# Optimization experiments

Measured on AMD Instinct MI355X. Metric: run time of the kernel, lower is better.

## Reference

```python
import jax, jax.numpy as jnp
import numpy as np

N_NODES = 100000
N_EDGES = 1600000
IN_C = 64
OUT_C = 64
BN_EPS = 1e-5


def setup_inputs() -> dict:
    key = jax.random.key(0)
    k1, k2, k3, k4 = jax.random.split(key, 4)
    x = jax.random.normal(k1, (N_NODES, IN_C), dtype=jnp.float32)
    edge_index = jax.random.randint(k2, (2, N_EDGES), 0, N_NODES, dtype=jnp.int64)
    # GCNConv linear: weight [out, in], bias [out] (PyG default has bias=True)
    W = jax.random.normal(k3, (OUT_C, IN_C), dtype=jnp.float32) / np.sqrt(IN_C)
    b = jax.random.normal(k4, (OUT_C,), dtype=jnp.float32) * 0.01
    # BatchNorm1d affine params
    gamma = jnp.ones((OUT_C,), dtype=jnp.float32)
    beta = jnp.zeros((OUT_C,), dtype=jnp.float32)
    return {"x": x, "edge_index": edge_index, "W": W, "b": b, "gamma": gamma, "beta": beta}


def reference(x, edge_index, W, b, gamma, beta):
    N = x.shape[0]
    # GCNConv: linear transform (no bias yet)
    h = x @ W.T  # [N, out]
    # add self-loops
    loop = jnp.arange(N, dtype=edge_index.dtype)
    src = jnp.concatenate([edge_index[0], loop])  # [E+N]
    dst = jnp.concatenate([edge_index[1], loop])
    # symmetric normalization: deg computed on destination (col)
    ones = jnp.ones(src.shape[0], dtype=h.dtype)
    deg = jax.ops.segment_sum(ones, dst, num_segments=N)  # [N]
    deg_inv_sqrt = jnp.where(deg > 0, jax.lax.rsqrt(deg), 0.0)
    norm = deg_inv_sqrt[src] * deg_inv_sqrt[dst]  # [E+N]
    # gather -> scale -> scatter-add aggregation
    msgs = h[src] * norm[:, None]  # [E+N, out] (dominant memory traffic)
    out = jax.ops.segment_sum(msgs, dst, num_segments=N) + b  # [N, out]
    # BatchNorm1d (training mode: biased batch statistics over nodes)
    mean = out.mean(axis=0)
    var = out.var(axis=0)  # biased, matching torch BN normalization
    y = (out - mean) * jax.lax.rsqrt(var + BN_EPS) * gamma + beta
    return jax.nn.relu(y)
```

## Files before the change

### kernel.cpp

```cpp
#include <hip/hip_runtime.h>
#include <math.h>

#define N_NODES 100000
#define N_EDGES 1600000
#define C 64
#define BN_EPS 1e-5f
#define SLOTS 48

#define WS_HP    0
#define WS_CNT   3200000
#define WS_STAT  3300000
#define WS_SLOT  3300128

#define NPART 8
#define PART_NODES (N_NODES / NPART)
#define NCHUNK 128
#define CHUNK_I4 (N_EDGES / 4 / NCHUNK)

static __device__ __forceinline__ unsigned short f2bf(float f) {
    unsigned u = __float_as_uint(f);
    unsigned r = 0x7FFFu + ((u >> 16) & 1u);
    return (unsigned short)((u + r) >> 16);
}
static __device__ __forceinline__ float bf2f(unsigned short h) {
    return __uint_as_float(((unsigned)h) << 16);
}

__global__ void r10_init(unsigned* __restrict__ cnt, float* __restrict__ stats) {
    int i = blockIdx.x * blockDim.x + threadIdx.x;
    if (i < N_NODES) cnt[i] = 0u;
    if (i < 128) stats[i] = 0.0f;
}

__global__ void r10_scatter(const int* __restrict__ ei, unsigned* __restrict__ cnt,
                            unsigned* __restrict__ slot) {
    const int p  = blockIdx.x & (NPART - 1);
    const int ch = blockIdx.x >> 3;
    const unsigned lo = (unsigned)(p * PART_NODES);
    const unsigned hi = lo + PART_NODES;
    const int4* d4 = reinterpret_cast<const int4*>(ei + N_EDGES);
    const int beg = ch * CHUNK_I4;
    const int end = beg + CHUNK_I4;
    for (int e = beg + threadIdx.x; e < end; e += 256) {
        int4 d = d4[e];
        unsigned dx = (unsigned)d.x, dy = (unsigned)d.y;
        unsigned dz = (unsigned)d.z, dw = (unsigned)d.w;
        if (dx >= lo && dx < hi) {
            unsigned s = (unsigned)ei[4 * e + 0];
            unsigned pos = atomicAdd(&cnt[dx], 1u);
            if (pos < SLOTS) slot[dx * SLOTS + pos] = s;
        }
        if (dy >= lo && dy < hi) {
            unsigned s = (unsigned)ei[4 * e + 1];
            unsigned pos = atomicAdd(&cnt[dy], 1u);
            if (pos < SLOTS) slot[dy * SLOTS + pos] = s;
        }
        if (dz >= lo && dz < hi) {
            unsigned s = (unsigned)ei[4 * e + 2];
            unsigned pos = atomicAdd(&cnt[dz], 1u);
            if (pos < SLOTS) slot[dz * SLOTS + pos] = s;
        }
        if (dw >= lo && dw < hi) {
            unsigned s = (unsigned)ei[4 * e + 3];
            unsigned pos = atomicAdd(&cnt[dw], 1u);
            if (pos < SLOTS) slot[dw * SLOTS + pos] = s;
        }
    }
}

__global__ void r10_mm(const float* __restrict__ x, const float* __restrict__ W,
                       const unsigned* __restrict__ cnt, unsigned short* __restrict__ hp) {
    __shared__ float Wt[64 * 64];
    __shared__ float X[16 * 64];
    const int tid = threadIdx.x;
    for (int i = tid; i < 64 * 64; i += 256)
        Wt[i] = W[((i & 63) << 6) + (i >> 6)];

    const int c = tid & 63;
    const int w = tid >> 6;
    const int nrow = tid >> 4;
    const int k4 = (tid & 15) << 2;
    const int ngroups = N_NODES / 16;

    for (int g = blockIdx.x; g < ngroups; g += gridDim.x) {
        const int base = g * 16;
        __syncthreads();
        *reinterpret_cast<float4*>(X + nrow * 64 + k4) =
            *reinterpret_cast<const float4*>(x + (base + nrow) * 64 + k4);
        __syncthreads();

        float acc0 = 0.f, acc1 = 0.f, acc2 = 0.f, acc3 = 0.f;
        #pragma unroll
        for (int k = 0; k < 64; k += 4) {
            float w0 = Wt[(k + 0) * 64 + c];
            float w1 = Wt[(k + 1) * 64 + c];
            float w2 = Wt[(k + 2) * 64 + c];
            float w3 = Wt[(k + 3) * 64 + c];
            float4 x0 = *reinterpret_cast<const float4*>(X + (w * 4 + 0) * 64 + k);
            float4 x1 = *reinterpret_cast<const float4*>(X + (w * 4 + 1) * 64 + k);
            float4 x2 = *reinterpret_cast<const float4*>(X + (w * 4 + 2) * 64 + k);
            float4 x3 = *reinterpret_cast<const float4*>(X + (w * 4 + 3) * 64 + k);
            acc0 += x0.x * w0 + x0.y * w1 + x0.z * w2 + x0.w * w3;
            acc1 += x1.x * w0 + x1.y * w1 + x1.z * w2 + x1.w * w3;
            acc2 += x2.x * w0 + x2.y * w1 + x2.z * w2 + x2.w * w3;
            acc3 += x3.x * w0 + x3.y * w1 + x3.z * w2 + x3.w * w3;
        }
        const int n0 = base + w * 4;
        hp[(n0 + 0) * 64 + c] = f2bf(acc0 * rsqrtf((float)(cnt[n0 + 0] + 1u)));
        hp[(n0 + 1) * 64 + c] = f2bf(acc1 * rsqrtf((float)(cnt[n0 + 1] + 1u)));
        hp[(n0 + 2) * 64 + c] = f2bf(acc2 * rsqrtf((float)(cnt[n0 + 2] + 1u)));
        hp[(n0 + 3) * 64 + c] = f2bf(acc3 * rsqrtf((float)(cnt[n0 + 3] + 1u)));
    }
}

__global__ void r10_agg(const unsigned* __restrict__ slot, const unsigned* __restrict__ cnt,
                        const unsigned short* __restrict__ hp, float* __restrict__ out,
                        float* __restrict__ stats) {
    __shared__ float ls[256], lq[256];
    const int tid = threadIdx.x;
    const int c = tid & 63;
    int wid = blockIdx.x * (blockDim.x >> 6) + (tid >> 6);
    const int nw = gridDim.x * (blockDim.x >> 6);
    float s = 0.0f, q = 0.0f;
    for (int n = wid; n < N_NODES; n += nw) {
        unsigned deg = cnt[n];
        int num = (deg > SLOTS) ? SLOTS : (int)deg;
        float dn = rsqrtf((float)(deg + 1u));
        float acc = bf2f(hp[n * 64 + c]);
        unsigned p = (c < num) ? slot[n * SLOTS + c] : 0u;
        int j = 0;
        for (; j + 8 <= num; j += 8) {
            unsigned s0 = __shfl(p, j + 0), s1 = __shfl(p, j + 1);
            unsigned s2 = __shfl(p, j + 2), s3 = __shfl(p, j + 3);
            unsigned s4 = __shfl(p, j + 4), s5 = __shfl(p, j + 5);
            unsigned s6 = __shfl(p, j + 6), s7 = __shfl(p, j + 7);
            float a0 = bf2f(hp[s0 * 64 + c]);
            float a1 = bf2f(hp[s1 * 64 + c]);
            float a2 = bf2f(hp[s2 * 64 + c]);
            float a3 = bf2f(hp[s3 * 64 + c]);
            float a4 = bf2f(hp[s4 * 64 + c]);
            float a5 = bf2f(hp[s5 * 64 + c]);
            float a6 = bf2f(hp[s6 * 64 + c]);
            float a7 = bf2f(hp[s7 * 64 + c]);
            acc += ((a0 + a1) + (a2 + a3)) + ((a4 + a5) + (a6 + a7));
        }
        for (; j + 4 <= num; j += 4) {
            unsigned s0 = __shfl(p, j + 0), s1 = __shfl(p, j + 1);
            unsigned s2 = __shfl(p, j + 2), s3 = __shfl(p, j + 3);
            float a0 = bf2f(hp[s0 * 64 + c]);
            float a1 = bf2f(hp[s1 * 64 + c]);
            float a2 = bf2f(hp[s2 * 64 + c]);
            float a3 = bf2f(hp[s3 * 64 + c]);
            acc += (a0 + a1) + (a2 + a3);
        }
        for (; j < num; ++j)
            acc += bf2f(hp[__shfl(p, j) * 64 + c]);
        float o = acc * dn;
        out[n * 64 + c] = o;
        s += o; q += o * o;
    }
    ls[tid] = s; lq[tid] = q;
    __syncthreads();
    if (tid < 64) {
        s = ls[tid] + ls[tid + 64] + ls[tid + 128] + ls[tid + 192];
        q = lq[tid] + lq[tid + 64] + lq[tid + 128] + lq[tid + 192];
        atomicAdd(&stats[tid], s);
        atomicAdd(&stats[64 + tid], q);
    }
}

__global__ void r10_bnrelu(float* __restrict__ out, const float* __restrict__ sum,
                           const float* __restrict__ sq, const float* __restrict__ gamma,
                           const float* __restrict__ beta) {
    int i = blockIdx.x * blockDim.x + threadIdx.x;
    const int st = gridDim.x * blockDim.x;
    const int c0 = (i & 15) << 2;
    float scl[4], sft[4];
    #pragma unroll
    for (int k = 0; k < 4; ++k) {
        float mean = sum[c0 + k] * (1.0f / N_NODES);
        float var  = sq[c0 + k] * (1.0f / N_NODES) - mean * mean;
        float inv  = rsqrtf(var + BN_EPS);
        scl[k] = gamma[c0 + k] * inv;
        sft[k] = beta[c0 + k] - mean * scl[k];
    }
    const int total4 = N_NODES * C / 4;
    for (; i < total4; i += st) {
        float4 v = reinterpret_cast<float4*>(out)[i];
        v.x = fmaxf(v.x * scl[0] + sft[0], 0.0f);
        v.y = fmaxf(v.y * scl[1] + sft[1], 0.0f);
        v.z = fmaxf(v.z * scl[2] + sft[2], 0.0f);
        v.w = fmaxf(v.w * scl[3] + sft[3], 0.0f);
        reinterpret_cast<float4*>(out)[i] = v;
    }
}

extern "C" void kernel_launch(void* const* d_in, const int* in_sizes, int n_in,
                              void* d_out, int out_size, void* d_ws, size_t ws_size,
                              hipStream_t stream) {
    const float* x     = (const float*)d_in[0];
    const int*   ei    = (const int*)d_in[1];
    const float* W     = (const float*)d_in[2];
    const float* gamma = (const float*)d_in[4];
    const float* beta  = (const float*)d_in[5];
    float* out = (float*)d_out;
    float*    wsf = (float*)d_ws;
    unsigned* wsu = (unsigned*)d_ws;

    unsigned short* hp = (unsigned short*)(wsf + WS_HP);
    unsigned* cnt   = wsu + WS_CNT;
    float*    stats = wsf + WS_STAT;
    unsigned* slot  = wsu + WS_SLOT;

    r10_init   <<<(N_NODES + 255) / 256, 256, 0, stream>>>(cnt, stats);
    r10_scatter<<<NPART * NCHUNK, 256, 0, stream>>>(ei, cnt, slot);
    r10_mm     <<<2048, 256, 0, stream>>>(x, W, cnt, hp);
    r10_agg    <<<4096, 256, 0, stream>>>(slot, cnt, hp, out, stats);
    r10_bnrelu <<<1024, 256, 0, stream>>>(out, stats, stats + 64, gamma, beta);
}
```

Before: 241.1 us.

## Gather two bf16 channels per lane across half-wave edge split in aggregation

The aggregation kernel now has each half of a wavefront process alternate neighbor edges, with each lane loading a 4-byte pair of bf16 channels instead of one 2-byte value. The two halves are then combined through shuffles. This halves the number of gather load instructions per edge and widens each access. Separately, the weight transpose in the matmul kernel gets a padded LDS layout with coalesced global reads, the output stores and loads in the final passes use nontemporal hints, and the bnrelu grid is doubled. The cost is extra shuffles and select operations per node, and a different floating-point summation order.

Measured after the change: 240.1 us. About the same (-0.4%).

```diff
diff --git a/kernel.cpp b/kernel.cpp
--- a/kernel.cpp
+++ b/kernel.cpp
@@ -17,6 +17,8 @@
 #define NCHUNK 128
 #define CHUNK_I4 (N_EDGES / 4 / NCHUNK)
 
+typedef float f4 __attribute__((ext_vector_type(4)));
+
 static __device__ __forceinline__ unsigned short f2bf(float f) {
     unsigned u = __float_as_uint(f);
     unsigned r = 0x7FFFu + ((u >> 16) & 1u);
@@ -26,13 +28,13 @@
     return __uint_as_float(((unsigned)h) << 16);
 }
 
-__global__ void r10_init(unsigned* __restrict__ cnt, float* __restrict__ stats) {
+__global__ void r20_init(unsigned* __restrict__ cnt, float* __restrict__ stats) {
     int i = blockIdx.x * blockDim.x + threadIdx.x;
     if (i < N_NODES) cnt[i] = 0u;
     if (i < 128) stats[i] = 0.0f;
 }
 
-__global__ void r10_scatter(const int* __restrict__ ei, unsigned* __restrict__ cnt,
+__global__ void r20_scatter(const int* __restrict__ ei, unsigned* __restrict__ cnt,
                             unsigned* __restrict__ slot) {
     const int p  = blockIdx.x & (NPART - 1);
     const int ch = blockIdx.x >> 3;
@@ -68,13 +70,15 @@
     }
 }
 
-__global__ void r10_mm(const float* __restrict__ x, const float* __restrict__ W,
+__global__ void r20_mm(const float* __restrict__ x, const float* __restrict__ W,
                        const unsigned* __restrict__ cnt, unsigned short* __restrict__ hp) {
-    __shared__ float Wt[64 * 64];
+    __shared__ float Wt[64 * 65];
     __shared__ float X[16 * 64];
     const int tid = threadIdx.x;
-    for (int i = tid; i < 64 * 64; i += 256)
-        Wt[i] = W[((i & 63) << 6) + (i >> 6)];
+    for (int i = tid; i < 64 * 64; i += 256) {
+        float v = W[i];
+        Wt[(i & 63) * 65 + (i >> 6)] = v;
+    }
 
     const int c = tid & 63;
     const int w = tid >> 6;
@@ -92,10 +96,10 @@
         float acc0 = 0.f, acc1 = 0.f, acc2 = 0.f, acc3 = 0.f;
         #pragma unroll
         for (int k = 0; k < 64; k += 4) {
-            float w0 = Wt[(k + 0) * 64 + c];
-            float w1 = Wt[(k + 1) * 64 + c];
-            float w2 = Wt[(k + 2) * 64 + c];
-            float w3 = Wt[(k + 3) * 64 + c];
+            float w0 = Wt[(k + 0) * 65 + c];
+            float w1 = Wt[(k + 1) * 65 + c];
+            float w2 = Wt[(k + 2) * 65 + c];
+            float w3 = Wt[(k + 3) * 65 + c];
             float4 x0 = *reinterpret_cast<const float4*>(X + (w * 4 + 0) * 64 + k);
             float4 x1 = *reinterpret_cast<const float4*>(X + (w * 4 + 1) * 64 + k);
             float4 x2 = *reinterpret_cast<const float4*>(X + (w * 4 + 2) * 64 + k);
@@ -113,50 +117,58 @@
     }
 }
 
-__global__ void r10_agg(const unsigned* __restrict__ slot, const unsigned* __restrict__ cnt,
+__global__ void r20_agg(const unsigned* __restrict__ slot, const unsigned* __restrict__ cnt,
                         const unsigned short* __restrict__ hp, float* __restrict__ out,
                         float* __restrict__ stats) {
     __shared__ float ls[256], lq[256];
     const int tid = threadIdx.x;
     const int c = tid & 63;
-    int wid = blockIdx.x * (blockDim.x >> 6) + (tid >> 6);
-    const int nw = gridDim.x * (blockDim.x >> 6);
+    const int half = c >> 5;
+    const int l2 = (c & 31) * 2;
+    int wid = blockIdx.x * 4 + (tid >> 6);
+    const int nw = gridDim.x * 4;
     float s = 0.0f, q = 0.0f;
     for (int n = wid; n < N_NODES; n += nw) {
         unsigned deg = cnt[n];
         int num = (deg > SLOTS) ? SLOTS : (int)deg;
         float dn = rsqrtf((float)(deg + 1u));
-        float acc = bf2f(hp[n * 64 + c]);
         unsigned p = (c < num) ? slot[n * SLOTS + c] : 0u;
+        float alo = 0.f, ahi = 0.f;
         int j = 0;
         for (; j + 8 <= num; j += 8) {
-            unsigned s0 = __shfl(p, j + 0), s1 = __shfl(p, j + 1);
-            unsigned s2 = __shfl(p, j + 2), s3 = __shfl(p, j + 3);
-            unsigned s4 = __shfl(p, j + 4), s5 = __shfl(p, j + 5);
-            unsigned s6 = __shfl(p, j + 6), s7 = __shfl(p, j + 7);
-            float a0 = bf2f(hp[s0 * 64 + c]);
-            float a1 = bf2f(hp[s1 * 64 + c]);
-            float a2 = bf2f(hp[s2 * 64 + c]);
-            float a3 = bf2f(hp[s3 * 64 + c]);
-            float a4 = bf2f(hp[s4 * 64 + c]);
-            float a5 = bf2f(hp[s5 * 64 + c]);
-            float a6 = bf2f(hp[s6 * 64 + c]);
-            float a7 = bf2f(hp[s7 * 64 + c]);
-            acc += ((a0 + a1) + (a2 + a3)) + ((a4 + a5) + (a6 + a7));
-        }
-        for (; j + 4 <= num; j += 4) {
-            unsigned s0 = __shfl(p, j + 0), s1 = __shfl(p, j + 1);
-            unsigned s2 = __shfl(p, j + 2), s3 = __shfl(p, j + 3);
-            float a0 = bf2f(hp[s0 * 64 + c]);
-            float a1 = bf2f(hp[s1 * 64 + c]);
-            float a2 = bf2f(hp[s2 * 64 + c]);
-            float a3 = bf2f(hp[s3 * 64 + c]);
-            acc += (a0 + a1) + (a2 + a3);
-        }
-        for (; j < num; ++j)
-            acc += bf2f(hp[__shfl(p, j) * 64 + c]);
-        float o = acc * dn;
-        out[n * 64 + c] = o;
+            unsigned r0e = __shfl(p, j + 0), r0o = __shfl(p, j + 1);
+            unsigned r1e = __shfl(p, j + 2), r1o = __shfl(p, j + 3);
+            unsigned r2e = __shfl(p, j + 4), r2o = __shfl(p, j + 5);
+            unsigned r3e = __shfl(p, j + 6), r3o = __shfl(p, j + 7);
+            unsigned r0 = half ? r0o : r0e;
+            unsigned r1 = half ? r1o : r1e;
+            unsigned r2 = half ? r2o : r2e;
+            unsigned r3 = half ? r3o : r3e;
+            ushort2 v0 = *reinterpret_cast<const ushort2*>(hp + r0 * 64 + l2);
+            ushort2 v1 = *reinterpret_cast<const ushort2*>(hp + r1 * 64 + l2);
+            ushort2 v2 = *reinterpret_cast<const ushort2*>(hp + r2 * 64 + l2);
+            ushort2 v3 = *reinterpret_cast<const ushort2*>(hp + r3 * 64 + l2);
+            alo += (bf2f(v0.x) + bf2f(v1.x)) + (bf2f(v2.x) + bf2f(v3.x));
+            ahi += (bf2f(v0.y) + bf2f(v1.y)) + (bf2f(v2.y) + bf2f(v3.y));
+        }
+        for (; j + 2 <= num; j += 2) {
+            unsigned re = __shfl(p, j), ro = __shfl(p, j + 1);
+            unsigned r = half ? ro : re;
+            ushort2 v = *reinterpret_cast<const ushort2*>(hp + r * 64 + l2);
+            alo += bf2f(v.x); ahi += bf2f(v.y);
+        }
+        if (j < num) {
+            unsigned re = __shfl(p, j);
+            ushort2 v = *reinterpret_cast<const ushort2*>(hp + re * 64 + l2);
+            if (half == 0) { alo += bf2f(v.x); ahi += bf2f(v.y); }
+        }
+        float elo = __shfl(alo, c >> 1);
+        float ehi = __shfl(ahi, c >> 1);
+        float olo = __shfl(alo, 32 + (c >> 1));
+        float ohi = __shfl(ahi, 32 + (c >> 1));
+        float edges = (c & 1) ? (ehi + ohi) : (elo + olo);
+        float o = (edges + bf2f(hp[n * 64 + c])) * dn;
+        __builtin_nontemporal_store(o, &out[n * 64 + c]);
         s += o; q += o * o;
     }
     ls[tid] = s; lq[tid] = q;
@@ -169,7 +181,7 @@
     }
 }
 
-__global__ void r10_bnrelu(float* __restrict__ out, const float* __restrict__ sum,
+__global__ void r20_bnrelu(float* __restrict__ out, const float* __restrict__ sum,
                            const float* __restrict__ sq, const float* __restrict__ gamma,
                            const float* __restrict__ beta) {
     int i = blockIdx.x * blockDim.x + threadIdx.x;
@@ -185,13 +197,14 @@
         sft[k] = beta[c0 + k] - mean * scl[k];
     }
     const int total4 = N_NODES * C / 4;
+    f4* o4 = reinterpret_cast<f4*>(out);
     for (; i < total4; i += st) {
-        float4 v = reinterpret_cast<float4*>(out)[i];
+        f4 v = __builtin_nontemporal_load(&o4[i]);
         v.x = fmaxf(v.x * scl[0] + sft[0], 0.0f);
         v.y = fmaxf(v.y * scl[1] + sft[1], 0.0f);
         v.z = fmaxf(v.z * scl[2] + sft[2], 0.0f);
         v.w = fmaxf(v.w * scl[3] + sft[3], 0.0f);
-        reinterpret_cast<float4*>(out)[i] = v;
+        __builtin_nontemporal_store(v, &o4[i]);
     }
 }
 
@@ -212,9 +225,9 @@
     float*    stats = wsf + WS_STAT;
     unsigned* slot  = wsu + WS_SLOT;
 
-    r10_init   <<<(N_NODES + 255) / 256, 256, 0, stream>>>(cnt, stats);
-    r10_scatter<<<NPART * NCHUNK, 256, 0, stream>>>(ei, cnt, slot);
-    r10_mm     <<<2048, 256, 0, stream>>>(x, W, cnt, hp);
-    r10_agg    <<<4096, 256, 0, stream>>>(slot, cnt, hp, out, stats);
-    r10_bnrelu <<<1024, 256, 0, stream>>>(out, stats, stats + 64, gamma, beta);
-}
+    r20_init   <<<(N_NODES + 255) / 256, 256, 0, stream>>>(cnt, stats);
+    r20_scatter<<<NPART * NCHUNK, 256, 0, stream>>>(ei, cnt, slot);
+    r20_mm     <<<2048, 256, 0, stream>>>(x, W, cnt, hp);
+    r20_agg    <<<4096, 256, 0, stream>>>(slot, cnt, hp, out, stats);
+    r20_bnrelu <<<2048, 256, 0, stream>>>(out, stats, stats + 64, gamma, beta);
+}
```
